# Kernel optimization log

Measured on AMD Instinct MI355X. Metric: run time of the kernel, lower is better.

Reference implementation:

```python
import jax, jax.numpy as jnp
import numpy as np

N = 50000
E = 400000
IN_DIM = 128
OUT_DIM = 512
NUM_MASK = 15000


def _init_linear(key, din, dout):
    s = 1.0 / np.sqrt(din)
    return jax.random.uniform(key, (din, dout), jnp.float32, -s, s)


def setup_inputs() -> dict:
    key = jax.random.key(0)
    ks = jax.random.split(key, 20)
    attr = jax.random.normal(ks[0], (N, IN_DIM), jnp.float32)
    src = jax.random.randint(ks[1], (E,), 0, N, jnp.int32)
    dst = jax.random.randint(ks[2], (E,), 0, N, jnp.int32)
    mask_nodes = jax.random.randint(ks[3], (NUM_MASK,), 0, N, jnp.int32)
    mask_token = jnp.zeros((1, IN_DIM), jnp.float32)
    dims = [(IN_DIM, OUT_DIM), (OUT_DIM, OUT_DIM), (OUT_DIM, OUT_DIM), (OUT_DIM, IN_DIM)]
    params = {}
    for i, (din, dout) in enumerate(dims, start=1):
        params[f"w_self{i}"] = _init_linear(ks[3 * i + 1], din, dout)
        params[f"w_neigh{i}"] = _init_linear(ks[3 * i + 2], din, dout)
        params[f"b{i}"] = jnp.zeros((dout,), jnp.float32)
    return dict(attr=attr, mask_token=mask_token, src=src, dst=dst, mask_nodes=mask_nodes, **params)


def sage_conv(h, src, dst, w_self, w_neigh, b):
    # mean aggregation over in-neighbors (DGL SAGEConv, aggregator_type='mean')
    msg = h[src]                                              # [E, d]
    agg = jax.ops.segment_sum(msg, dst, num_segments=N)       # [N, d]
    deg = jax.ops.segment_sum(jnp.ones((E,), h.dtype), dst, num_segments=N)
    h_neigh = agg / jnp.maximum(deg, 1.0)[:, None]
    return h @ w_self + h_neigh @ w_neigh + b


def reference(attr, mask_token, src, dst, mask_nodes,
              w_self1, w_neigh1, b1, w_self2, w_neigh2, b2,
              w_self3, w_neigh3, b3, w_self4, w_neigh4, b4):
    # mask node features with the mask token
    h = attr.at[mask_nodes].set(mask_token[0])
    h = jax.nn.relu(sage_conv(h, src, dst, w_self1, w_neigh1, b1))
    h = sage_conv(h, src, dst, w_self2, w_neigh2, b2)          # encoded
    h = jax.nn.relu(sage_conv(h, src, dst, w_self3, w_neigh3, b3))
    decoded = sage_conv(h, src, dst, w_self4, w_neigh4, b4)
    x_orig = attr[mask_nodes]
    x_rec = decoded[mask_nodes]
    return jnp.mean((x_rec - x_orig) ** 2)
```

## Files before the change

### kernel.cpp

```cpp
#include <hip/hip_runtime.h>
#include <cstdint>
#include <cstddef>

#define IN_DIM 128
#define HID    512

typedef unsigned int   uint32;
typedef unsigned short u16;
typedef __attribute__((ext_vector_type(8))) short bf16x8;
typedef __attribute__((ext_vector_type(4))) float f32x4;

static inline int imin_h(int a, int b) { return a < b ? a : b; }

__device__ __forceinline__ float bfu2f(uint32 u) { return __uint_as_float(u << 16); }
__device__ __forceinline__ u16 f2bf(float f) {
  uint32 x = __float_as_uint(f);
  x += 0x7fffu + ((x >> 16) & 1u);
  return (u16)(x >> 16);
}
__device__ __forceinline__ uint32 pack2(float a, float b) {
  return (uint32)f2bf(a) | ((uint32)f2bf(b) << 16);
}

#define GLOBAL_AS(p) ((const __attribute__((address_space(1))) void*)(p))
#define LDS_AS(p)    ((__attribute__((address_space(3))) void*)(p))

__global__ void k_zero(int* __restrict__ p, int n) {
  for (int i = blockIdx.x * blockDim.x + threadIdx.x; i < n; i += gridDim.x * blockDim.x)
    p[i] = 0;
}

__global__ void k_hist(const int* __restrict__ dst, int* __restrict__ deg, int E) {
  for (int e = blockIdx.x * blockDim.x + threadIdx.x; e < E; e += gridDim.x * blockDim.x)
    atomicAdd(&deg[dst[e]], 1);
}

__global__ __launch_bounds__(256)
void k_scan1(const int* __restrict__ deg, int* __restrict__ bsum, int n) {
  __shared__ int sm[256];
  const int base = blockIdx.x * 2048 + threadIdx.x * 8;
  int s = 0;
  if (base + 8 <= n) {
    const uint4 a = *reinterpret_cast<const uint4*>(deg + base);
    const uint4 b = *reinterpret_cast<const uint4*>(deg + base + 4);
    s = (int)(a.x + a.y + a.z + a.w + b.x + b.y + b.z + b.w);
  } else {
    for (int i = 0; i < 8; ++i) if (base + i < n) s += deg[base + i];
  }
  sm[threadIdx.x] = s;
  __syncthreads();
  for (int off = 128; off > 0; off >>= 1) {
    if (threadIdx.x < off) sm[threadIdx.x] += sm[threadIdx.x + off];
    __syncthreads();
  }
  if (threadIdx.x == 0) bsum[blockIdx.x] = sm[0];
}

__global__ __launch_bounds__(256)
void k_scan2(int* __restrict__ bsum, int nb, int* __restrict__ rowptr, int n) {
  __shared__ int sm[256];
  const int v = (threadIdx.x < nb) ? bsum[threadIdx.x] : 0;
  sm[threadIdx.x] = v;
  __syncthreads();
  for (int off = 1; off < 256; off <<= 1) {
    const int t = (threadIdx.x >= off) ? sm[threadIdx.x - off] : 0;
    __syncthreads();
    sm[threadIdx.x] += t;
    __syncthreads();
  }
  if (threadIdx.x < nb) bsum[threadIdx.x] = sm[threadIdx.x] - v;
  if (threadIdx.x == nb - 1) rowptr[n] = sm[threadIdx.x];
}

__global__ __launch_bounds__(256)
void k_scan3(const int* __restrict__ deg, const int* __restrict__ bsum,
             int* __restrict__ rowptr, int* __restrict__ cursor, int n) {
  __shared__ int sm[256];
  const int base = blockIdx.x * 2048 + threadIdx.x * 8;
  int v[8];
  int s = 0;
#pragma unroll
  for (int i = 0; i < 8; ++i) {
    v[i] = (base + i < n) ? deg[base + i] : 0;
    s += v[i];
  }
  sm[threadIdx.x] = s;
  __syncthreads();
  for (int off = 1; off < 256; off <<= 1) {
    const int t = (threadIdx.x >= off) ? sm[threadIdx.x - off] : 0;
    __syncthreads();
    sm[threadIdx.x] += t;
    __syncthreads();
  }
  int run = bsum[blockIdx.x] + sm[threadIdx.x] - s;
#pragma unroll
  for (int i = 0; i < 8; ++i) {
    if (base + i < n) { rowptr[base + i] = run; cursor[base + i] = run; }
    run += v[i];
  }
}

__global__ void k_fill(const int* __restrict__ src, const int* __restrict__ dst,
                       int* __restrict__ cursor, int* __restrict__ col, int E) {
  for (int e = blockIdx.x * blockDim.x + threadIdx.x; e < E; e += gridDim.x * blockDim.x) {
    const int p = atomicAdd(&cursor[dst[e]], 1);
    col[p] = src[e];
  }
}

__global__ void k_cvt(const float4* __restrict__ in, uint2* __restrict__ out, int n4) {
  for (int i = blockIdx.x * blockDim.x + threadIdx.x; i < n4; i += gridDim.x * blockDim.x) {
    const float4 v = in[i];
    out[i] = make_uint2(pack2(v.x, v.y), pack2(v.z, v.w));
  }
}

__global__ void k_mask(const float4* __restrict__ token, const int* __restrict__ mask,
                       uint2* __restrict__ h0, int NM) {
  const int total = NM * (IN_DIM / 4);
  for (int i = blockIdx.x * blockDim.x + threadIdx.x; i < total; i += gridDim.x * blockDim.x) {
    const int m = i >> 5;
    const int c = i & 31;
    const float4 t = token[c];
    h0[(size_t)mask[m] * (IN_DIM / 4) + c] = make_uint2(pack2(t.x, t.y), pack2(t.z, t.w));
  }
}

__global__ void k_wt(const float* __restrict__ W, u16* __restrict__ Wt, int K, int Nn) {
  const int total = K * Nn;
  for (int t = blockIdx.x * blockDim.x + threadIdx.x; t < total; t += gridDim.x * blockDim.x) {
    const int n = t / K, k = t - n * K;
    const size_t idx = ((size_t)(n >> 4) * (K >> 5) + (k >> 5)) * 512 +
                       ((k >> 3) & 3) * 128 + ((n & 15) << 3) + (k & 7);
    Wt[idx] = f2bf(W[(size_t)k * Nn + n]);
  }
}

template <int D, bool REMAP>
__global__ __launch_bounds__(256)
void k_agg(const u16* __restrict__ h, const int* __restrict__ col,
           const int* __restrict__ rowptr, const int* __restrict__ nodes,
           u16* __restrict__ out, int n) {
  constexpr int V = D / 64;
  const int w = blockIdx.x * (blockDim.x >> 6) + (threadIdx.x >> 6);
  if (w >= n) return;
  const int node = REMAP ? nodes[w] : w;
  const int lane = threadIdx.x & 63;
  const int beg = rowptr[node], end = rowptr[node + 1];
  const size_t loff = (size_t)lane * V;
  float acc[V];
#pragma unroll
  for (int j = 0; j < V; ++j) acc[j] = 0.f;
  if constexpr (V == 8) {
    uint4 cur;
    if (beg < end) cur = *reinterpret_cast<const uint4*>(h + (size_t)col[beg] * D + loff);
    for (int e = beg; e < end; ++e) {
      uint4 nxt = cur;
      if (e + 1 < end)
        nxt = *reinterpret_cast<const uint4*>(h + (size_t)col[e + 1] * D + loff);
      acc[0] += bfu2f(cur.x & 0xffffu); acc[1] += bfu2f(cur.x >> 16);
      acc[2] += bfu2f(cur.y & 0xffffu); acc[3] += bfu2f(cur.y >> 16);
      acc[4] += bfu2f(cur.z & 0xffffu); acc[5] += bfu2f(cur.z >> 16);
      acc[6] += bfu2f(cur.w & 0xffffu); acc[7] += bfu2f(cur.w >> 16);
      cur = nxt;
    }
  } else {
    uint32 cur = 0;
    if (beg < end) cur = *reinterpret_cast<const uint32*>(h + (size_t)col[beg] * D + loff);
    for (int e = beg; e < end; ++e) {
      uint32 nxt = cur;
      if (e + 1 < end)
        nxt = *reinterpret_cast<const uint32*>(h + (size_t)col[e + 1] * D + loff);
      acc[0] += bfu2f(cur & 0xffffu); acc[1] += bfu2f(cur >> 16);
      cur = nxt;
    }
  }
  const float inv = 1.0f / fmaxf((float)(end - beg), 1.0f);
  u16* o = out + (size_t)w * D + loff;
  if constexpr (V == 8) {
    uint4 u;
    u.x = pack2(acc[0] * inv, acc[1] * inv);
    u.y = pack2(acc[2] * inv, acc[3] * inv);
    u.z = pack2(acc[4] * inv, acc[5] * inv);
    u.w = pack2(acc[6] * inv, acc[7] * inv);
    *reinterpret_cast<uint4*>(o) = u;
  } else {
    *reinterpret_cast<uint32*>(o) = pack2(acc[0] * inv, acc[1] * inv);
  }
}

template <int DIN, bool RELU>
__global__ __launch_bounds__(512, 4)
void k_gemm_big(const u16* __restrict__ A1, const u16* __restrict__ A2,
                const u16* __restrict__ Wt1, const u16* __restrict__ Wt2,
                const float* __restrict__ bias, u16* __restrict__ out, int M) {
  constexpr int DOUT = HID;
  __shared__ char lds[73728];
  constexpr int KS = DIN / 32;
  constexpr int S  = 2 * KS;
  const int tid = threadIdx.x;
  const int w = tid >> 6, l = tid & 63;
  const int l15 = l & 15, l4 = l >> 4;
  const int wm = w >> 2, wn = w & 3;

  const int nwg  = gridDim.x * gridDim.y;
  const int orig = blockIdx.x + gridDim.x * blockIdx.y;
  const int q = nwg >> 3, r = nwg & 7;
  const int xcd = orig & 7, seq = orig >> 3;
  const int wg = (xcd < r ? xcd * (q + 1) : r * (q + 1) + (xcd - r) * q) + seq;
  const int mt = wg >> 1, nt = wg & 1;
  const int m0 = mt * 128, n0 = nt * 256;

  f32x4 acc[4][4];
#pragma unroll
  for (int i = 0; i < 4; ++i)
#pragma unroll
    for (int j = 0; j < 4; ++j) acc[i][j] = (f32x4){0.f, 0.f, 0.f, 0.f};

  const int arow = min(m0 + w * 16 + l15, M - 1);
  const int kl = l4 * 8;
  const u16* pA1 = A1 + (size_t)arow * DIN + kl;
  const u16* pA2 = A2 + (size_t)arow * DIN + kl;
  const u16* bb1 = Wt1 + ((size_t)(n0 >> 4) + 2 * w) * KS * 512 + (size_t)l * 8;
  const u16* bb2 = Wt2 + ((size_t)(n0 >> 4) + 2 * w) * KS * 512 + (size_t)l * 8;

  auto stage = [&](int s) {
    const int ph = s / KS;
    const int kf = s - ph * KS;
    char* buf = lds + (s % 3) * 24576;
    const u16* a0 = (ph ? pA2 : pA1) + kf * 32;
    const u16* b0 = (ph ? bb2 : bb1) + kf * 512;
    const u16* b1 = b0 + KS * 512;
    __builtin_amdgcn_global_load_lds(GLOBAL_AS(a0), LDS_AS(buf + w * 1024), 16, 0, 0);
    __builtin_amdgcn_global_load_lds(GLOBAL_AS(b0), LDS_AS(buf + 8192 + (2 * w + 0) * 1024), 16, 0, 0);
    __builtin_amdgcn_global_load_lds(GLOBAL_AS(b1), LDS_AS(buf + 8192 + (2 * w + 1) * 1024), 16, 0, 0);
  };

  stage(0);
  stage(1);

#pragma unroll
  for (int s = 0; s < S; ++s) {
    if (s + 1 < S) asm volatile("s_waitcnt vmcnt(3)" ::: "memory");
    else           asm volatile("s_waitcnt vmcnt(0)" ::: "memory");
    __builtin_amdgcn_s_barrier();
    if (s + 2 < S) stage(s + 2);
    char* buf = lds + (s % 3) * 24576;
    bf16x8 af[4], bfr[4];
#pragma unroll
    for (int i = 0; i < 4; ++i)
      af[i] = *reinterpret_cast<const bf16x8*>(buf + (wm * 4 + i) * 1024 + l * 16);
#pragma unroll
    for (int j = 0; j < 4; ++j)
      bfr[j] = *reinterpret_cast<const bf16x8*>(buf + 8192 + (wn * 4 + j) * 1024 + l * 16);
#pragma unroll
    for (int i = 0; i < 4; ++i)
#pragma unroll
      for (int j = 0; j < 4; ++j)
        acc[i][j] = __builtin_amdgcn_mfma_f32_16x16x32_bf16(af[i], bfr[j], acc[i][j], 0, 0, 0);
    asm volatile("s_waitcnt lgkmcnt(0)" ::: "memory");
  }
  __builtin_amdgcn_s_barrier();

  u16* eb = (u16*)(lds + w * 9216);
  float bv[4];
#pragma unroll
  for (int j = 0; j < 4; ++j) bv[j] = bias[n0 + wn * 64 + j * 16 + l15];
#pragma unroll
  for (int i = 0; i < 4; ++i)
#pragma unroll
    for (int j = 0; j < 4; ++j)
#pragma unroll
      for (int r = 0; r < 4; ++r) {
        const int lr = i * 16 + l4 * 4 + r;
        float t = acc[i][j][r] + bv[j];
        if (RELU) t = fmaxf(t, 0.f);
        eb[lr * 72 + j * 16 + l15] = f2bf(t);
      }
  asm volatile("s_waitcnt lgkmcnt(0)" ::: "memory");
#pragma unroll
  for (int p = 0; p < 8; ++p) {
    const int lr = p * 8 + (l >> 3);
    const int row = m0 + wm * 64 + lr;
    if (row < M) {
      const uint4 v = *reinterpret_cast<const uint4*>(eb + lr * 72 + (l & 7) * 8);
      *reinterpret_cast<uint4*>(out + (size_t)row * DOUT + n0 + wn * 64 + (l & 7) * 8) = v;
    }
  }
}

template <int DIN, int DOUT, bool RELU, bool REMAP>
__global__ __launch_bounds__(256, 3)
void k_gemm(const u16* __restrict__ A1, const u16* __restrict__ A2,
            const u16* __restrict__ Wt1, const u16* __restrict__ Wt2,
            const float* __restrict__ bias, u16* __restrict__ out, int M,
            const int* __restrict__ remap) {
  __shared__ char lds[49152];
  constexpr int KS = DIN / 32;
  constexpr int S  = 2 * KS;
  const int tid = threadIdx.x;
  const int w = tid >> 6, l = tid & 63;
  const int l15 = l & 15, l4 = l >> 4;
  const int wm = w >> 1, wn = w & 1;

  const int nwg  = gridDim.x * gridDim.y;
  const int orig = blockIdx.x + gridDim.x * blockIdx.y;
  const int q = nwg >> 3, r = nwg & 7;
  const int xcd = orig & 7, seq = orig >> 3;
  const int wg = (xcd < r ? xcd * (q + 1) : r * (q + 1) + (xcd - r) * q) + seq;
  constexpr int NT = DOUT / 128;
  const int mt = wg / NT, nt = wg - mt * NT;
  const int m0 = mt * 128, n0 = nt * 128;

  f32x4 acc[4][4];
#pragma unroll
  for (int i = 0; i < 4; ++i)
#pragma unroll
    for (int j = 0; j < 4; ++j) acc[i][j] = (f32x4){0.f, 0.f, 0.f, 0.f};

  const int am0 = min(m0 + (2 * w) * 16 + l15, M - 1);
  const int am1 = min(m0 + (2 * w + 1) * 16 + l15, M - 1);
  const int ar0 = REMAP ? remap[am0] : am0;
  const int ar1 = REMAP ? remap[am1] : am1;
  const int kl = l4 * 8;
  const u16* pA1r0 = A1 + (size_t)ar0 * DIN + kl;
  const u16* pA1r1 = A1 + (size_t)ar1 * DIN + kl;
  const u16* pA2r0 = A2 + (size_t)am0 * DIN + kl;
  const u16* pA2r1 = A2 + (size_t)am1 * DIN + kl;
  const u16* bb1 = Wt1 + ((size_t)(n0 >> 4) + 2 * w) * KS * 512 + (size_t)l * 8;
  const u16* bb2 = Wt2 + ((size_t)(n0 >> 4) + 2 * w) * KS * 512 + (size_t)l * 8;

  auto stage = [&](int s) {
    const int ph = s / KS;
    const int kf = s - ph * KS;
    char* buf = lds + (s % 3) * 16384;
    const u16* a0 = (ph ? pA2r0 : pA1r0) + kf * 32;
    const u16* a1 = (ph ? pA2r1 : pA1r1) + kf * 32;
    const u16* b0 = (ph ? bb2 : bb1) + kf * 512;
    const u16* b1 = b0 + KS * 512;
    __builtin_amdgcn_global_load_lds(GLOBAL_AS(a0), LDS_AS(buf + (2 * w + 0) * 1024), 16, 0, 0);
    __builtin_amdgcn_global_load_lds(GLOBAL_AS(a1), LDS_AS(buf + (2 * w + 1) * 1024), 16, 0, 0);
    __builtin_amdgcn_global_load_lds(GLOBAL_AS(b0), LDS_AS(buf + 8192 + (2 * w + 0) * 1024), 16, 0, 0);
    __builtin_amdgcn_global_load_lds(GLOBAL_AS(b1), LDS_AS(buf + 8192 + (2 * w + 1) * 1024), 16, 0, 0);
  };

  stage(0);
  stage(1);

#pragma unroll
  for (int s = 0; s < S; ++s) {
    if (s + 1 < S) asm volatile("s_waitcnt vmcnt(4)" ::: "memory");
    else           asm volatile("s_waitcnt vmcnt(0)" ::: "memory");
    __builtin_amdgcn_s_barrier();
    if (s + 2 < S) stage(s + 2);
    char* buf = lds + (s % 3) * 16384;
    bf16x8 af[4], bfr[4];
#pragma unroll
    for (int i = 0; i < 4; ++i)
      af[i] = *reinterpret_cast<const bf16x8*>(buf + (wm * 4 + i) * 1024 + l * 16);
#pragma unroll
    for (int j = 0; j < 4; ++j)
      bfr[j] = *reinterpret_cast<const bf16x8*>(buf + 8192 + (wn * 4 + j) * 1024 + l * 16);
#pragma unroll
    for (int i = 0; i < 4; ++i)
#pragma unroll
      for (int j = 0; j < 4; ++j)
        acc[i][j] = __builtin_amdgcn_mfma_f32_16x16x32_bf16(af[i], bfr[j], acc[i][j], 0, 0, 0);
    asm volatile("s_waitcnt lgkmcnt(0)" ::: "memory");
  }

#pragma unroll
  for (int j = 0; j < 4; ++j) {
    const int c = n0 + wn * 64 + j * 16 + l15;
    const float bv = bias[c];
#pragma unroll
    for (int i = 0; i < 4; ++i) {
      const int rowb = m0 + wm * 64 + i * 16 + l4 * 4;
#pragma unroll
      for (int r = 0; r < 4; ++r) {
        const int row = rowb + r;
        if (row < M) {
          float t = acc[i][j][r] + bv;
          if (RELU) t = fmaxf(t, 0.f);
          out[(size_t)row * DOUT + c] = f2bf(t);
        }
      }
    }
  }
}

__global__ __launch_bounds__(256)
void k_loss1(const u16* __restrict__ dec, const float* __restrict__ attr,
             const int* __restrict__ mask, int NM, float* __restrict__ partials) {
  __shared__ float sm[256];
  float s = 0.f;
  const int total = NM * (IN_DIM / 4);
  for (int idx = blockIdx.x * blockDim.x + threadIdx.x; idx < total; idx += gridDim.x * blockDim.x) {
    const int m = idx >> 5, c = (idx & 31) * 4;
    const int node = mask[m];
    const float4 a = *reinterpret_cast<const float4*>(&attr[(size_t)node * IN_DIM + c]);
    const uint2 d2 = *reinterpret_cast<const uint2*>(&dec[(size_t)m * IN_DIM + c]);
    const float dx = bfu2f(d2.x & 0xffffu) - a.x;
    const float dy = bfu2f(d2.x >> 16)     - a.y;
    const float dz = bfu2f(d2.y & 0xffffu) - a.z;
    const float dw = bfu2f(d2.y >> 16)     - a.w;
    s += dx * dx + dy * dy + dz * dz + dw * dw;
  }
  sm[threadIdx.x] = s;
  __syncthreads();
  for (int off = 128; off > 0; off >>= 1) {
    if (threadIdx.x < off) sm[threadIdx.x] += sm[threadIdx.x + off];
    __syncthreads();
  }
  if (threadIdx.x == 0) partials[blockIdx.x] = sm[0];
}

__global__ __launch_bounds__(256)
void k_loss2(const float* __restrict__ partials, int nb, float* __restrict__ out, float inv) {
  __shared__ float sm[256];
  float s = 0.f;
  for (int i = threadIdx.x; i < nb; i += 256) s += partials[i];
  sm[threadIdx.x] = s;
  __syncthreads();
  for (int off = 128; off > 0; off >>= 1) {
    if (threadIdx.x < off) sm[threadIdx.x] += sm[threadIdx.x + off];
    __syncthreads();
  }
  if (threadIdx.x == 0) out[0] = sm[0] * inv;
}

extern "C" void kernel_launch(void* const* d_in, const int* in_sizes, int n_in,
                              void* d_out, int out_size, void* d_ws, size_t ws_size,
                              hipStream_t stream) {
  const float* attr  = (const float*)d_in[0];
  const float* token = (const float*)d_in[1];
  const int*   src   = (const int*)d_in[2];
  const int*   dst   = (const int*)d_in[3];
  const int*   mask  = (const int*)d_in[4];
  const float* Wself[4]  = {(const float*)d_in[5], (const float*)d_in[8],
                            (const float*)d_in[11], (const float*)d_in[14]};
  const float* Wneigh[4] = {(const float*)d_in[6], (const float*)d_in[9],
                            (const float*)d_in[12], (const float*)d_in[15]};
  const float* Bias[4]   = {(const float*)d_in[7], (const float*)d_in[10],
                            (const float*)d_in[13], (const float*)d_in[16]};
  const int N  = in_sizes[0] / IN_DIM;
  const int E  = in_sizes[2];
  const int NM = in_sizes[4];

  size_t off = 0;
  auto take = [&](size_t bytes) -> void* {
    void* p = (char*)d_ws + off;
    off += (bytes + 255) & ~(size_t)255;
    return p;
  };
  u16* HA = (u16*)take((size_t)N * HID * sizeof(u16));
  u16* HB = (u16*)take((size_t)N * HID * sizeof(u16));
  const int dims_in[4]  = {IN_DIM, HID, HID, HID};
  const int dims_out[4] = {HID, HID, HID, IN_DIM};
  u16* WtS[4]; u16* WtN[4];
  for (int i = 0; i < 4; ++i) {
    WtS[i] = (u16*)take((size_t)dims_in[i] * dims_out[i] * sizeof(u16));
    WtN[i] = (u16*)take((size_t)dims_in[i] * dims_out[i] * sizeof(u16));
  }
  int* deg    = (int*)take((size_t)N * sizeof(int));
  int* rowptr = (int*)take((size_t)(N + 1) * sizeof(int));
  int* cursor = (int*)take((size_t)N * sizeof(int));
  int* col    = (int*)take((size_t)E * sizeof(int));
  int* bsum   = (int*)take(256 * sizeof(int));
  float* partials = (float*)take(512 * sizeof(float));

  size_t rem = (ws_size > off + 4096) ? (ws_size - off - 4096) : 0;
  const int cap = (int)(rem / ((size_t)HID * sizeof(u16)));
  const int want = (N + 255) & ~255;
  int chunk = (cap >= want) ? want : (cap & ~255);
  if (chunk < 2048) chunk = 2048;
  u16* CH = (u16*)take((size_t)chunk * HID * sizeof(u16));
  u16* DEC = HA;

  k_zero<<<imin_h((N + 255) / 256, 1024), 256, 0, stream>>>(deg, N);
  const int eb = imin_h((E + 255) / 256, 4096);
  k_hist<<<eb, 256, 0, stream>>>(dst, deg, E);
  const int nb = (N + 2047) / 2048;
  k_scan1<<<nb, 256, 0, stream>>>(deg, bsum, N);
  k_scan2<<<1, 256, 0, stream>>>(bsum, nb, rowptr, N);
  k_scan3<<<nb, 256, 0, stream>>>(deg, bsum, rowptr, cursor, N);
  k_fill<<<eb, 256, 0, stream>>>(src, dst, cursor, col, E);

  for (int i = 0; i < 4; ++i) {
    const int tot = dims_in[i] * dims_out[i];
    k_wt<<<imin_h((tot + 255) / 256, 2048), 256, 0, stream>>>(Wself[i],  WtS[i], dims_in[i], dims_out[i]);
    k_wt<<<imin_h((tot + 255) / 256, 2048), 256, 0, stream>>>(Wneigh[i], WtN[i], dims_in[i], dims_out[i]);
  }

  const int n4 = N * (IN_DIM / 4);
  k_cvt<<<imin_h((n4 + 255) / 256, 2048), 256, 0, stream>>>((const float4*)attr, (uint2*)HA, n4);
  k_mask<<<imin_h((NM * (IN_DIM / 4) + 255) / 256, 2048), 256, 0, stream>>>(
      (const float4*)token, mask, (uint2*)HA, NM);

  auto run_layer = [&](const u16* hin, u16* hout, int din, int layer, bool relu) {
    for (int c0 = 0; c0 < N; c0 += chunk) {
      const int mc = imin_h(chunk, N - c0);
      const int ab = (mc + 3) / 4;
      if (din == IN_DIM)
        k_agg<IN_DIM, false><<<ab, 256, 0, stream>>>(hin, col, rowptr + c0, nullptr, CH, mc);
      else
        k_agg<HID, false><<<ab, 256, 0, stream>>>(hin, col, rowptr + c0, nullptr, CH, mc);
      const u16* a1 = hin + (size_t)c0 * din;
      u16* o = hout + (size_t)c0 * HID;
      const int mb = (mc + 127) / 128;
      if (din == IN_DIM && relu)
        k_gemm_big<IN_DIM, true><<<dim3(2, mb), 512, 0, stream>>>(
            a1, CH, WtS[layer], WtN[layer], Bias[layer], o, mc);
      else if (relu)
        k_gemm_big<HID, true><<<dim3(2, mb), 512, 0, stream>>>(
            a1, CH, WtS[layer], WtN[layer], Bias[layer], o, mc);
      else
        k_gemm_big<HID, false><<<dim3(2, mb), 512, 0, stream>>>(
            a1, CH, WtS[layer], WtN[layer], Bias[layer], o, mc);
    }
  };

  run_layer(HA, HB, IN_DIM, 0, true);
  run_layer(HB, HA, HID,    1, false);
  run_layer(HA, HB, HID,    2, true);

  k_agg<HID, true><<<(NM + 3) / 4, 256, 0, stream>>>(HB, col, rowptr, mask, CH, NM);
  k_gemm<HID, IN_DIM, false, true><<<dim3(1, (NM + 127) / 128), 256, 0, stream>>>(
      HB, CH, WtS[3], WtN[3], Bias[3], DEC, NM, mask);

  k_loss1<<<512, 256, 0, stream>>>(DEC, attr, mask, NM, partials);
  k_loss2<<<1, 256, 0, stream>>>(partials, 512, (float*)d_out, 1.0f / ((float)NM * IN_DIM));
}
```

Baseline: 455.6 us.

## Fuse aggregation and GEMM into one launch, software-pipelined across node chunks

Each layer is split into four node chunks. A single kernel launch now runs the GEMM for chunk t-1 alongside the neighbor aggregation for chunk t, with separate blocks assigned to each role and two chunk buffers alternating. The aim is to overlap the memory-bound gather with the compute-bound GEMM and to cut down on launch boundaries. In exchange, aggregation blocks now use 512 threads and share a kernel with a large LDS allocation, occupancy bounds drop to 2, and there is one extra pipeline stage per layer.

```diff
diff --git a/kernel.cpp b/kernel.cpp
--- a/kernel.cpp
+++ b/kernel.cpp
@@ -136,17 +136,10 @@
   }
 }
 
-template <int D, bool REMAP>
-__global__ __launch_bounds__(256)
-void k_agg(const u16* __restrict__ h, const int* __restrict__ col,
-           const int* __restrict__ rowptr, const int* __restrict__ nodes,
-           u16* __restrict__ out, int n) {
+template <int D>
+__device__ __forceinline__ void agg_node(const u16* __restrict__ h, const int* __restrict__ col,
+                                         int beg, int end, int lane, u16* __restrict__ orow) {
   constexpr int V = D / 64;
-  const int w = blockIdx.x * (blockDim.x >> 6) + (threadIdx.x >> 6);
-  if (w >= n) return;
-  const int node = REMAP ? nodes[w] : w;
-  const int lane = threadIdx.x & 63;
-  const int beg = rowptr[node], end = rowptr[node + 1];
   const size_t loff = (size_t)lane * V;
   float acc[V];
 #pragma unroll
@@ -176,7 +169,7 @@
     }
   }
   const float inv = 1.0f / fmaxf((float)(end - beg), 1.0f);
-  u16* o = out + (size_t)w * D + loff;
+  u16* o = orow + loff;
   if constexpr (V == 8) {
     uint4 u;
     u.x = pack2(acc[0] * inv, acc[1] * inv);
@@ -189,22 +182,49 @@
   }
 }
 
+template <int D, bool REMAP>
+__global__ __launch_bounds__(256)
+void k_agg(const u16* __restrict__ h, const int* __restrict__ col,
+           const int* __restrict__ rowptr, const int* __restrict__ nodes,
+           u16* __restrict__ out, int n) {
+  const int w = blockIdx.x * (blockDim.x >> 6) + (threadIdx.x >> 6);
+  if (w >= n) return;
+  const int node = REMAP ? nodes[w] : w;
+  agg_node<D>(h, col, rowptr[node], rowptr[node + 1], threadIdx.x & 63,
+              out + (size_t)w * D);
+}
+
 template <int DIN, bool RELU>
-__global__ __launch_bounds__(512, 4)
-void k_gemm_big(const u16* __restrict__ A1, const u16* __restrict__ A2,
-                const u16* __restrict__ Wt1, const u16* __restrict__ Wt2,
-                const float* __restrict__ bias, u16* __restrict__ out, int M) {
+__global__ __launch_bounds__(512, 2)
+void k_fused(const u16* __restrict__ hfull,
+             const u16* __restrict__ A1,
+             const u16* __restrict__ A2,
+             u16* __restrict__ CHout,
+             const int* __restrict__ col,
+             const int* __restrict__ rowptr_c,
+             const u16* __restrict__ Wt1, const u16* __restrict__ Wt2,
+             const float* __restrict__ bias,
+             u16* __restrict__ out,
+             int n_agg, int M, int gemm_blocks) {
   constexpr int DOUT = HID;
   __shared__ char lds[73728];
   constexpr int KS = DIN / 32;
   constexpr int S  = 2 * KS;
   const int tid = threadIdx.x;
   const int w = tid >> 6, l = tid & 63;
+
+  if ((int)blockIdx.x >= gemm_blocks) {
+    const int wl = ((int)blockIdx.x - gemm_blocks) * 8 + w;
+    if (wl >= n_agg) return;
+    agg_node<DIN>(hfull, col, rowptr_c[wl], rowptr_c[wl + 1], l, CHout + (size_t)wl * DIN);
+    return;
+  }
+
   const int l15 = l & 15, l4 = l >> 4;
   const int wm = w >> 2, wn = w & 3;
 
-  const int nwg  = gridDim.x * gridDim.y;
-  const int orig = blockIdx.x + gridDim.x * blockIdx.y;
+  const int nwg  = gemm_blocks;
+  const int orig = blockIdx.x;
   const int q = nwg >> 3, r = nwg & 7;
   const int xcd = orig & 7, seq = orig >> 3;
   const int wg = (xcd < r ? xcd * (q + 1) : r * (q + 1) + (xcd - r) * q) + seq;
@@ -271,9 +291,9 @@
 #pragma unroll
     for (int j = 0; j < 4; ++j)
 #pragma unroll
-      for (int r = 0; r < 4; ++r) {
-        const int lr = i * 16 + l4 * 4 + r;
-        float t = acc[i][j][r] + bv[j];
+      for (int r2 = 0; r2 < 4; ++r2) {
+        const int lr = i * 16 + l4 * 4 + r2;
+        float t = acc[i][j][r2] + bv[j];
         if (RELU) t = fmaxf(t, 0.f);
         eb[lr * 72 + j * 16 + l15] = f2bf(t);
       }
@@ -377,10 +397,10 @@
     for (int i = 0; i < 4; ++i) {
       const int rowb = m0 + wm * 64 + i * 16 + l4 * 4;
 #pragma unroll
-      for (int r = 0; r < 4; ++r) {
-        const int row = rowb + r;
+      for (int r2 = 0; r2 < 4; ++r2) {
+        const int row = rowb + r2;
         if (row < M) {
-          float t = acc[i][j][r] + bv;
+          float t = acc[i][j][r2] + bv;
           if (RELU) t = fmaxf(t, 0.f);
           out[(size_t)row * DOUT + c] = f2bf(t);
         }
@@ -469,12 +489,13 @@
   int* bsum   = (int*)take(256 * sizeof(int));
   float* partials = (float*)take(512 * sizeof(float));
 
-  size_t rem = (ws_size > off + 4096) ? (ws_size - off - 4096) : 0;
-  const int cap = (int)(rem / ((size_t)HID * sizeof(u16)));
-  const int want = (N + 255) & ~255;
-  int chunk = (cap >= want) ? want : (cap & ~255);
-  if (chunk < 2048) chunk = 2048;
-  u16* CH = (u16*)take((size_t)chunk * HID * sizeof(u16));
+  const int C = 4;
+  int cstart[C + 1];
+  const int cbase = ((N / C) + 255) & ~255;
+  for (int i = 0; i <= C; ++i) cstart[i] = imin_h(i * cbase, N);
+  u16* CH0 = (u16*)take((size_t)cbase * HID * sizeof(u16));
+  u16* CH1 = (u16*)take((size_t)cbase * HID * sizeof(u16));
+  u16* CHp[2] = {CH0, CH1};
   u16* DEC = HA;
 
   k_zero<<<imin_h((N + 255) / 256, 1024), 256, 0, stream>>>(deg, N);
@@ -498,25 +519,31 @@
       (const float4*)token, mask, (uint2*)HA, NM);
 
   auto run_layer = [&](const u16* hin, u16* hout, int din, int layer, bool relu) {
-    for (int c0 = 0; c0 < N; c0 += chunk) {
-      const int mc = imin_h(chunk, N - c0);
-      const int ab = (mc + 3) / 4;
+    for (int t = 0; t <= C; ++t) {
+      const int a0 = (t < C) ? cstart[t] : 0;
+      const int an = (t < C) ? (cstart[t + 1] - cstart[t]) : 0;
+      const int g0 = (t > 0) ? cstart[t - 1] : 0;
+      const int gm = (t > 0) ? (cstart[t] - cstart[t - 1]) : 0;
+      const int gb = (t > 0) ? ((gm + 127) / 128) * 2 : 0;
+      const int ab = (an + 7) / 8;
+      const int total = gb + ab;
+      if (total == 0) continue;
+      u16* cha = CHp[t & 1];
+      const u16* chg = CHp[(t ^ 1) & 1];
+      const u16* a1 = hin + (size_t)g0 * din;
+      u16* o = hout + (size_t)g0 * HID;
       if (din == IN_DIM)
-        k_agg<IN_DIM, false><<<ab, 256, 0, stream>>>(hin, col, rowptr + c0, nullptr, CH, mc);
+        k_fused<IN_DIM, true><<<total, 512, 0, stream>>>(
+            hin, a1, chg, cha, col, rowptr + a0,
+            WtS[layer], WtN[layer], Bias[layer], o, an, gm, gb);
+      else if (relu)
+        k_fused<HID, true><<<total, 512, 0, stream>>>(
+            hin, a1, chg, cha, col, rowptr + a0,
+            WtS[layer], WtN[layer], Bias[layer], o, an, gm, gb);
       else
-        k_agg<HID, false><<<ab, 256, 0, stream>>>(hin, col, rowptr + c0, nullptr, CH, mc);
-      const u16* a1 = hin + (size_t)c0 * din;
-      u16* o = hout + (size_t)c0 * HID;
-      const int mb = (mc + 127) / 128;
-      if (din == IN_DIM && relu)
-        k_gemm_big<IN_DIM, true><<<dim3(2, mb), 512, 0, stream>>>(
-            a1, CH, WtS[layer], WtN[layer], Bias[layer], o, mc);
-      else if (relu)
-        k_gemm_big<HID, true><<<dim3(2, mb), 512, 0, stream>>>(
-            a1, CH, WtS[layer], WtN[layer], Bias[layer], o, mc);
-      else
-        k_gemm_big<HID, false><<<dim3(2, mb), 512, 0, stream>>>(
-            a1, CH, WtS[layer], WtN[layer], Bias[layer], o, mc);
+        k_fused<HID, false><<<total, 512, 0, stream>>>(
+            hin, a1, chg, cha, col, rowptr + a0,
+            WtS[layer], WtN[layer], Bias[layer], o, an, gm, gb);
     }
   };
 
@@ -524,9 +551,9 @@
   run_layer(HB, HA, HID,    1, false);
   run_layer(HA, HB, HID,    2, true);
 
-  k_agg<HID, true><<<(NM + 3) / 4, 256, 0, stream>>>(HB, col, rowptr, mask, CH, NM);
+  k_agg<HID, true><<<(NM + 3) / 4, 256, 0, stream>>>(HB, col, rowptr, mask, CH0, NM);
   k_gemm<HID, IN_DIM, false, true><<<dim3(1, (NM + 127) / 128), 256, 0, stream>>>(
-      HB, CH, WtS[3], WtN[3], Bias[3], DEC, NM, mask);
+      HB, CH0, WtS[3], WtN[3], Bias[3], DEC, NM, mask);
 
   k_loss1<<<512, 256, 0, stream>>>(DEC, attr, mask, NM, partials);
   k_loss2<<<1, 256, 0, stream>>>(partials, 512, (float*)d_out, 1.0f / ((float)NM * IN_DIM));
```

After: 707.2 us. +55.2%, slower.
